# Kernel tuning notes

Hardware: AMD Instinct MI355X
Metric: run time of the kernel (lower is better)

## Reference

```python
import jax, jax.numpy as jnp
import numpy as np

VOCAB = 100000
EMB = 256
HID = 512
H = HID // 2            # per-direction hidden size
T_LEN = 2048
N_TAGS = 7
START, END = 5, 6
NEG = -10000.0


def setup_inputs() -> dict:
    key = jax.random.key(0)
    ks = jax.random.split(key, 16)
    n = lambda k, sh: jax.random.normal(k, sh, dtype=jnp.float32)
    bound = 1.0 / np.sqrt(H)  # torch LSTM/Linear-style init scale
    u = lambda k, sh: jax.random.uniform(k, sh, dtype=jnp.float32, minval=-bound, maxval=bound)
    transitions = n(ks[12], (N_TAGS, N_TAGS))
    transitions = transitions.at[:, START].set(NEG).at[END, :].set(NEG)
    return {
        "words": jax.random.randint(ks[0], (T_LEN,), 0, VOCAB),
        "embed": n(ks[1], (VOCAB + 1, EMB)),
        "W_ih_f": u(ks[2], (4 * H, EMB)),
        "W_hh_f": u(ks[3], (4 * H, H)),
        "b_ih_f": u(ks[4], (4 * H,)),
        "b_hh_f": u(ks[5], (4 * H,)),
        "W_ih_b": u(ks[6], (4 * H, EMB)),
        "W_hh_b": u(ks[7], (4 * H, H)),
        "b_ih_b": u(ks[8], (4 * H,)),
        "b_hh_b": u(ks[9], (4 * H,)),
        "W_out": u(ks[10], (N_TAGS, HID)),
        "b_out": u(ks[11], (N_TAGS,)),
        "transitions": transitions,
        "h0": n(ks[13], (2, H)),
        "c0": n(ks[14], (2, H)),
    }


def _lstm_dir(xs, h0, c0, Wih, Whh, bih, bhh):
    # xs: [T, EMB]; torch gate order i, f, g, o
    def step(carry, x):
        h, c = carry
        g = x @ Wih.T + bih + h @ Whh.T + bhh  # [4H]
        i, f, gg, o = jnp.split(g, 4)
        i, f, o = jax.nn.sigmoid(i), jax.nn.sigmoid(f), jax.nn.sigmoid(o)
        c = f * c + i * jnp.tanh(gg)
        h = o * jnp.tanh(c)
        return (h, c), h
    _, hs = jax.lax.scan(step, (h0, c0), xs)
    return hs  # [T, H]


def _features(words, embed, W_ih_f, W_hh_f, b_ih_f, b_hh_f,
              W_ih_b, W_hh_b, b_ih_b, b_hh_b, W_out, b_out, h0, c0):
    xs = embed[words]                                   # [T, EMB]
    hs_f = _lstm_dir(xs, h0[0], c0[0], W_ih_f, W_hh_f, b_ih_f, b_hh_f)
    hs_b = _lstm_dir(xs[::-1], h0[1], c0[1], W_ih_b, W_hh_b, b_ih_b, b_hh_b)[::-1]
    lstm_out = jnp.concatenate([hs_f, hs_b], axis=1)    # [T, HID]
    return lstm_out @ W_out.T + b_out                   # [T, N_TAGS]


def _viterbi(feats, transitions):
    init = jnp.full((N_TAGS,), NEG, dtype=feats.dtype).at[START].set(0.0)

    def vit_step(fv, feat):
        # torch code: next_tag_var[j] = forward_var + transitions[j]
        M = fv[None, :] + transitions          # [j, i] = fv[i] + T[j, i]
        bp = jnp.argmax(M, axis=1)             # [N_TAGS] best prev tag
        fv_new = jnp.max(M, axis=1) + feat
        return fv_new, bp

    fv, bptrs = jax.lax.scan(vit_step, init, feats)     # bptrs: [T, N_TAGS]
    terminal = fv + transitions[END]
    final_tag = jnp.argmax(terminal)
    path_score = terminal[final_tag]

    def back_step(tag, bp):
        return bp[tag], tag
    _start, path = jax.lax.scan(back_step, final_tag, bptrs, reverse=True)
    return path_score, path  # path: [T] tag ids (B/I/E/S/N = 0..4)


def reference(words, embed, W_ih_f, W_hh_f, b_ih_f, b_hh_f,
              W_ih_b, W_hh_b, b_ih_b, b_hh_b, W_out, b_out,
              transitions, h0, c0):
    feats = _features(words, embed, W_ih_f, W_hh_f, b_ih_f, b_hh_f,
                      W_ih_b, W_hh_b, b_ih_b, b_hh_b, W_out, b_out, h0, c0)
    return _viterbi(feats, transitions)
```

## Files before the change

kernel.cpp:

```cpp
#include <hip/hip_runtime.h>

typedef unsigned int u32;

#define T_LEN 2048
#define NEG (-10000.0f)
#define WSCALE 2032.0f
#define HSCALE 127.0f
#define SCALE_INV (1.0f / (2032.0f * 127.0f))

__device__ __forceinline__ int sdot4(u32 a, u32 b, int c) {
#if __has_builtin(__builtin_amdgcn_sdot4)
  return __builtin_amdgcn_sdot4((int)a, (int)b, c, false);
#else
  int r = c;
  r += (int)(signed char)(a)       * (int)(signed char)(b);
  r += (int)(signed char)(a >> 8)  * (int)(signed char)(b >> 8);
  r += (int)(signed char)(a >> 16) * (int)(signed char)(b >> 16);
  r += (int)(signed char)(a >> 24) * (int)(signed char)(b >> 24);
  return r;
#endif
}

__device__ __forceinline__ u32 rdlane_u32(u32 v, int lane) {
#if __has_builtin(__builtin_amdgcn_readlane)
  return (u32)__builtin_amdgcn_readlane((int)v, lane);
#else
  return (u32)__shfl((int)v, lane);
#endif
}

__device__ __forceinline__ float rdlane_f32(float v, int lane) {
  return __builtin_bit_cast(float, rdlane_u32(__builtin_bit_cast(u32, v), lane));
}

__global__ void pack_whh_i8(const float* __restrict__ Wf,
                            const float* __restrict__ Wb,
                            u32* __restrict__ WP) {
  int idx = blockIdx.x * 256 + threadIdx.x;
  int d   = idx >> 16;
  int rem = idx & 65535;
  int q   = rem >> 12;
  int r   = (rem >> 2) & 1023;
  int j   = rem & 3;
  const float* W = d ? Wb : Wf;
  float4 v = *(const float4*)&W[r * 256 + q * 16 + j * 4];
  int b0 = (int)rintf(fminf(fmaxf(v.x * WSCALE, -127.f), 127.f));
  int b1 = (int)rintf(fminf(fmaxf(v.y * WSCALE, -127.f), 127.f));
  int b2 = (int)rintf(fminf(fmaxf(v.z * WSCALE, -127.f), 127.f));
  int b3 = (int)rintf(fminf(fmaxf(v.w * WSCALE, -127.f), 127.f));
  WP[((d * 16 + q) * 1024 + r) * 4 + j] =
      (u32)(b0 & 255) | ((u32)(b1 & 255) << 8) |
      ((u32)(b2 & 255) << 16) | ((u32)(b3 & 255) << 24);
}

__global__ void gather_kernel(const int* __restrict__ words,
                              const float* __restrict__ embed,
                              float* __restrict__ xs) {
  int t = blockIdx.x;
  int k = threadIdx.x;
  xs[t * 256 + k] = embed[(size_t)words[t] * 256 + k];
}

__global__ __launch_bounds__(256) void gemm_xw(
    const float* __restrict__ xs,
    const float* __restrict__ Wf, const float* __restrict__ Wb,
    const float* __restrict__ bihf, const float* __restrict__ bhhf,
    const float* __restrict__ bihb, const float* __restrict__ bhhb,
    float* __restrict__ XW) {
  __shared__ float lx[32 * 256];
  __shared__ float lw[32 * 132];
  const int tid = threadIdx.x;
  const int t0 = blockIdx.x * 32;
  const int g0 = blockIdx.y * 128;
  const int d  = blockIdx.z;
  const float* W = d ? Wb : Wf;

  #pragma unroll 4
  for (int r = 0; r < 32; ++r) lx[r * 256 + tid] = xs[(t0 + r) * 256 + tid];

  const int tg = tid & 31, tt = tid >> 5;
  float acc[4][4] = {};

  for (int kc = 0; kc < 8; ++kc) {
    __syncthreads();
    #pragma unroll
    for (int r2 = 0; r2 < 16; ++r2) {
      int gg = r2 * 8 + (tid >> 5);
      int k  = tid & 31;
      lw[k * 132 + gg] = W[(g0 + gg) * 256 + kc * 32 + k];
    }
    __syncthreads();
    #pragma unroll
    for (int k = 0; k < 32; ++k) {
      float4 wv = *(const float4*)&lw[k * 132 + tg * 4];
      #pragma unroll
      for (int a = 0; a < 4; ++a) {
        float xa = lx[(tt * 4 + a) * 256 + kc * 32 + k];
        acc[a][0] = fmaf(xa, wv.x, acc[a][0]);
        acc[a][1] = fmaf(xa, wv.y, acc[a][1]);
        acc[a][2] = fmaf(xa, wv.z, acc[a][2]);
        acc[a][3] = fmaf(xa, wv.w, acc[a][3]);
      }
    }
  }
  const float* bih = d ? bihb : bihf;
  const float* bhh = d ? bhhb : bhhf;
  int gcol = g0 + tg * 4;
  float4 bb;
  bb.x = bih[gcol + 0] + bhh[gcol + 0];
  bb.y = bih[gcol + 1] + bhh[gcol + 1];
  bb.z = bih[gcol + 2] + bhh[gcol + 2];
  bb.w = bih[gcol + 3] + bhh[gcol + 3];
  #pragma unroll
  for (int a = 0; a < 4; ++a) {
    float4 o;
    o.x = acc[a][0] + bb.x;
    o.y = acc[a][1] + bb.y;
    o.z = acc[a][2] + bb.z;
    o.w = acc[a][3] + bb.w;
    *(float4*)&XW[((size_t)d * T_LEN + t0 + tt * 4 + a) * 1024 + gcol] = o;
  }
}

__global__ void __launch_bounds__(512)
__attribute__((amdgpu_waves_per_eu(2, 2)))
lstm_seq(
    const float* __restrict__ XW, float* __restrict__ HS,
    const u32* __restrict__ wpack,
    const float* __restrict__ h0, const float* __restrict__ c0) {
  __shared__ u32   H8[64];
  __shared__ float GT[1024];
  const int tid = threadIdx.x;
  const int d = blockIdx.x;
  const int lane = tid & 63;

  uint4 w0[16], w1[16];
  const uint4* wr = (const uint4*)wpack;
  #pragma unroll
  for (int q = 0; q < 16; ++q) {
    w0[q] = wr[(d * 16 + q) * 1024 + tid];
    w1[q] = wr[(d * 16 + q) * 1024 + tid + 512];
  }

  float c = 0.0f, h = 0.0f;
  if (tid < 256) {
    c = c0[d * 256 + tid];
    h = h0[d * 256 + tid];
    int hi = (int)rintf(fminf(fmaxf(h, -1.0f), 1.0f) * HSCALE);
    int h1v = __shfl_down(hi, 1);
    int h2v = __shfl_down(hi, 2);
    int h3v = __shfl_down(hi, 3);
    if (!(tid & 3))
      H8[tid >> 2] = (u32)(hi & 255) | ((u32)(h1v & 255) << 8) |
                     ((u32)(h2v & 255) << 16) | ((u32)(h3v & 255) << 24);
  }
  __syncthreads();
  u32 hA = H8[lane];

  const int delta = d ? -1024 : 1024;
  const float* xwp = XW + ((size_t)d * T_LEN + (d ? (T_LEN - 1) : 0)) * 1024 + tid;
  float xw0c = xwp[0], xw1c = xwp[512];

  for (int s = 0; s < T_LEN; ++s) {
    float xw0n = 0.0f, xw1n = 0.0f;
    if (s < T_LEN - 1) { xwp += delta; xw0n = xwp[0]; xw1n = xwp[512]; }

    int a0 = 0, b0 = 0;
    int a1 = 0, b1 = 0;
    #pragma unroll
    for (int q = 0; q < 16; ++q) {
      u32 s0 = rdlane_u32(hA, 4 * q + 0);
      u32 s1 = rdlane_u32(hA, 4 * q + 1);
      u32 s2 = rdlane_u32(hA, 4 * q + 2);
      u32 s3 = rdlane_u32(hA, 4 * q + 3);
      a0 = sdot4(w0[q].x, s0, a0);
      a1 = sdot4(w1[q].x, s0, a1);
      b0 = sdot4(w0[q].y, s1, b0);
      b1 = sdot4(w1[q].y, s1, b1);
      a0 = sdot4(w0[q].z, s2, a0);
      a1 = sdot4(w1[q].z, s2, a1);
      b0 = sdot4(w0[q].w, s3, b0);
      b1 = sdot4(w1[q].w, s3, b1);
    }
    GT[tid]       = fmaf((float)(a0 + b0), SCALE_INV, xw0c);
    GT[tid + 512] = fmaf((float)(a1 + b1), SCALE_INV, xw1c);
    __syncthreads();

    const int t = d ? (T_LEN - 1 - s) : s;
    if (tid < 256) {
      float gi = GT[tid];
      float gf = GT[256 + tid];
      float gc = GT[512 + tid];
      float go = GT[768 + tid];
      gi = 1.0f / (1.0f + __expf(-gi));
      gf = 1.0f / (1.0f + __expf(-gf));
      go = 1.0f / (1.0f + __expf(-go));
      gc = 1.0f - 2.0f / (__expf(2.0f * gc) + 1.0f);
      c = gf * c + gi * gc;
      float th = 1.0f - 2.0f / (__expf(2.0f * c) + 1.0f);
      h = go * th;
      HS[((size_t)d * T_LEN + t) * 256 + tid] = h;
      int hi = (int)rintf(h * HSCALE);
      int h1v = __shfl_down(hi, 1);
      int h2v = __shfl_down(hi, 2);
      int h3v = __shfl_down(hi, 3);
      if (!(tid & 3))
        H8[tid >> 2] = (u32)(hi & 255) | ((u32)(h1v & 255) << 8) |
                       ((u32)(h2v & 255) << 16) | ((u32)(h3v & 255) << 24);
    }
    __syncthreads();
    hA = H8[lane];
    xw0c = xw0n;
    xw1c = xw1n;
  }
}

__global__ void feats_kernel(const float* __restrict__ hs,
                             const float* __restrict__ wout,
                             const float* __restrict__ bout,
                             float* __restrict__ feats) {
  __shared__ float lf[16 * 257];
  __shared__ float lb[16 * 257];
  const int tid = threadIdx.x;
  const int t0 = blockIdx.x * 16;
  for (int i = tid; i < 16 * 256; i += 128) {
    int r = i >> 8, k = i & 255;
    lf[r * 257 + k] = hs[(size_t)(t0 + r) * 256 + k];
    lb[r * 257 + k] = hs[(size_t)T_LEN * 256 + (size_t)(t0 + r) * 256 + k];
  }
  __syncthreads();
  const int tl = tid >> 3, n = tid & 7;
  if (n < 7) {
    float acc = bout[n];
    #pragma unroll 8
    for (int k = 0; k < 256; ++k) acc = fmaf(lf[tl * 257 + k], wout[n * 512 + k], acc);
    #pragma unroll 8
    for (int k = 0; k < 256; ++k) acc = fmaf(lb[tl * 257 + k], wout[n * 512 + 256 + k], acc);
    feats[(t0 + tl) * 7 + n] = acc;
  }
}

__global__ __launch_bounds__(256) void viterbi_kernel(
    const float* __restrict__ feats,
    const float* __restrict__ trans,
    float* __restrict__ out) {
  extern __shared__ char vsm[];
  float*         fe = (float*)vsm;
  unsigned char* bp = (unsigned char*)(vsm + 57344);
  unsigned char* G  = (unsigned char*)(vsm + 73728);
  unsigned char* bt = (unsigned char*)(vsm + 73984);
  const int tid = threadIdx.x;

  for (int i = tid; i < T_LEN * 7; i += 256) fe[i] = feats[i];
  __syncthreads();

  if (tid < 64) {
    const int j  = tid;
    const int jc = (j < 7) ? j : 0;
    float Trow[7];
    #pragma unroll
    for (int i = 0; i < 7; ++i) Trow[i] = trans[jc * 7 + i];
    float fv = (j == 5) ? 0.0f : NEG;
    for (int t = 0; t < T_LEN; ++t) {
      float f0 = rdlane_f32(fv, 0), f1 = rdlane_f32(fv, 1), f2 = rdlane_f32(fv, 2),
            f3 = rdlane_f32(fv, 3), f4 = rdlane_f32(fv, 4), f5 = rdlane_f32(fv, 5),
            f6 = rdlane_f32(fv, 6);
      float v0 = f0 + Trow[0], v1 = f1 + Trow[1], v2 = f2 + Trow[2],
            v3 = f3 + Trow[3], v4 = f4 + Trow[4], v5 = f5 + Trow[5],
            v6 = f6 + Trow[6];
      bool c01 = v0 >= v1;  float m01 = c01 ? v0 : v1;  int i01 = c01 ? 0 : 1;
      bool c23 = v2 >= v3;  float m23 = c23 ? v2 : v3;  int i23 = c23 ? 2 : 3;
      bool c45 = v4 >= v5;  float m45 = c45 ? v4 : v5;  int i45 = c45 ? 4 : 5;
      bool cA  = m01 >= m23; float mA = cA ? m01 : m23; int iA = cA ? i01 : i23;
      bool cB  = m45 >= v6;  float mB = cB ? m45 : v6;  int iB = cB ? i45 : 6;
      bool cF  = mA >= mB;   float best = cF ? mA : mB; int bi = cF ? iA : iB;
      if (j < 7) bp[t * 8 + j] = (unsigned char)bi;
      fv = best + fe[t * 7 + jc];
    }
    float term = fv + trans[42 + jc];
    float best = rdlane_f32(term, 0); int btag = 0;
    #pragma unroll
    for (int i = 1; i < 7; ++i) {
      float ti = rdlane_f32(term, i);
      if (ti > best) { best = ti; btag = i; }
    }
    if (j == 0) {
      out[0] = best;
      bt[31] = (unsigned char)btag;
    }
  }
  __syncthreads();

  {
    const int s = tid >> 3, j = tid & 7;
    if (s < 32 && j < 7) {
      int g = j;
      for (int t = s * 64 + 63; t >= s * 64; --t) g = bp[t * 8 + g];
      G[s * 8 + j] = (unsigned char)g;
    }
  }
  __syncthreads();

  if (tid == 0) {
    int x = bt[31];
    for (int s = 31; s >= 1; --s) { x = G[s * 8 + x]; bt[s - 1] = (unsigned char)x; }
  }
  __syncthreads();

  if (tid < 32) {
    const int s = tid;
    int tag = bt[s];
    for (int t = s * 64 + 63; t >= s * 64; --t) {
      out[1 + t] = (float)tag;
      tag = bp[t * 8 + tag];
    }
  }
}

extern "C" void kernel_launch(void* const* d_in, const int* in_sizes, int n_in,
                              void* d_out, int out_size, void* d_ws, size_t ws_size,
                              hipStream_t stream) {
  const int*   words = (const int*)d_in[0];
  const float* embed = (const float*)d_in[1];
  const float* Wih_f = (const float*)d_in[2];
  const float* Whh_f = (const float*)d_in[3];
  const float* bih_f = (const float*)d_in[4];
  const float* bhh_f = (const float*)d_in[5];
  const float* Wih_b = (const float*)d_in[6];
  const float* Whh_b = (const float*)d_in[7];
  const float* bih_b = (const float*)d_in[8];
  const float* bhh_b = (const float*)d_in[9];
  const float* Wout  = (const float*)d_in[10];
  const float* bout  = (const float*)d_in[11];
  const float* trans = (const float*)d_in[12];
  const float* h0    = (const float*)d_in[13];
  const float* c0    = (const float*)d_in[14];

  float* ws = (float*)d_ws;
  float* XW = ws;
  float* HS = ws + 4194304;
  float* XS = ws + 5242880;
  float* FE = ws + 5767168;
  u32*   WP = (u32*)(ws + 5781504);

  pack_whh_i8<<<512, 256, 0, stream>>>(Whh_f, Whh_b, WP);
  gather_kernel<<<T_LEN, 256, 0, stream>>>(words, embed, XS);
  dim3 ggrid(T_LEN / 32, 1024 / 128, 2);
  gemm_xw<<<ggrid, 256, 0, stream>>>(XS, Wih_f, Wih_b, bih_f, bhh_f, bih_b, bhh_b, XW);
  lstm_seq<<<2, 512, 0, stream>>>(XW, HS, WP, h0, c0);
  feats_kernel<<<128, 128, 0, stream>>>(HS, Wout, bout, FE);
  viterbi_kernel<<<1, 256, 74048, stream>>>(FE, trans, (float*)d_out);
}
```

Before: 2.615 ms.

## Use byte LDS stores for h, inline-asm dot4 with SGPR operand, lighter barriers

Replaces the three shuffle-down ops and packing with direct per-thread byte stores into the shared int8 h buffer. The dot products become inline v_dot4_i32_i8 with the broadcast h word as a scalar operand, and readlanes are software-pipelined one group ahead. __syncthreads is replaced by an explicit lgkmcnt wait plus s_barrier so the barrier does not also wait on outstanding global (vmcnt) loads and stores. Together these shorten the serial per-timestep critical path of the recurrent loop, at the risk of the asm constraints limiting compiler scheduling.

```diff
diff --git a/kernel.cpp b/kernel.cpp
--- a/kernel.cpp
+++ b/kernel.cpp
@@ -8,18 +8,8 @@
 #define HSCALE 127.0f
 #define SCALE_INV (1.0f / (2032.0f * 127.0f))
 
-__device__ __forceinline__ int sdot4(u32 a, u32 b, int c) {
-#if __has_builtin(__builtin_amdgcn_sdot4)
-  return __builtin_amdgcn_sdot4((int)a, (int)b, c, false);
-#else
-  int r = c;
-  r += (int)(signed char)(a)       * (int)(signed char)(b);
-  r += (int)(signed char)(a >> 8)  * (int)(signed char)(b >> 8);
-  r += (int)(signed char)(a >> 16) * (int)(signed char)(b >> 16);
-  r += (int)(signed char)(a >> 24) * (int)(signed char)(b >> 24);
-  return r;
-#endif
-}
+#define DOT(acc, w, hs) \
+  asm("v_dot4_i32_i8 %0, %2, %1, %0" : "+v"(acc) : "v"(w), "s"(hs))
 
 __device__ __forceinline__ u32 rdlane_u32(u32 v, int lane) {
 #if __has_builtin(__builtin_amdgcn_readlane)
@@ -31,6 +21,11 @@
 
 __device__ __forceinline__ float rdlane_f32(float v, int lane) {
   return __builtin_bit_cast(float, rdlane_u32(__builtin_bit_cast(u32, v), lane));
+}
+
+__device__ __forceinline__ void block_sync_lds() {
+  asm volatile("s_waitcnt lgkmcnt(0)" ::: "memory");
+  __builtin_amdgcn_s_barrier();
 }
 
 __global__ void pack_whh_i8(const float* __restrict__ Wf,
@@ -147,14 +142,9 @@
     c = c0[d * 256 + tid];
     h = h0[d * 256 + tid];
     int hi = (int)rintf(fminf(fmaxf(h, -1.0f), 1.0f) * HSCALE);
-    int h1v = __shfl_down(hi, 1);
-    int h2v = __shfl_down(hi, 2);
-    int h3v = __shfl_down(hi, 3);
-    if (!(tid & 3))
-      H8[tid >> 2] = (u32)(hi & 255) | ((u32)(h1v & 255) << 8) |
-                     ((u32)(h2v & 255) << 16) | ((u32)(h3v & 255) << 24);
-  }
-  __syncthreads();
+    ((unsigned char*)H8)[tid] = (unsigned char)(hi & 255);
+  }
+  block_sync_lds();
   u32 hA = H8[lane];
 
   const int delta = d ? -1024 : 1024;
@@ -167,24 +157,34 @@
 
     int a0 = 0, b0 = 0;
     int a1 = 0, b1 = 0;
-    #pragma unroll
-    for (int q = 0; q < 16; ++q) {
-      u32 s0 = rdlane_u32(hA, 4 * q + 0);
-      u32 s1 = rdlane_u32(hA, 4 * q + 1);
-      u32 s2 = rdlane_u32(hA, 4 * q + 2);
-      u32 s3 = rdlane_u32(hA, 4 * q + 3);
-      a0 = sdot4(w0[q].x, s0, a0);
-      a1 = sdot4(w1[q].x, s0, a1);
-      b0 = sdot4(w0[q].y, s1, b0);
-      b1 = sdot4(w1[q].y, s1, b1);
-      a0 = sdot4(w0[q].z, s2, a0);
-      a1 = sdot4(w1[q].z, s2, a1);
-      b0 = sdot4(w0[q].w, s3, b0);
-      b1 = sdot4(w1[q].w, s3, b1);
+    {
+      u32 s0 = rdlane_u32(hA, 0);
+      u32 s1 = rdlane_u32(hA, 1);
+      u32 s2 = rdlane_u32(hA, 2);
+      u32 s3 = rdlane_u32(hA, 3);
+      #pragma unroll
+      for (int q = 0; q < 16; ++q) {
+        u32 n0 = 0, n1 = 0, n2 = 0, n3 = 0;
+        if (q < 15) {
+          n0 = rdlane_u32(hA, 4 * q + 4);
+          n1 = rdlane_u32(hA, 4 * q + 5);
+          n2 = rdlane_u32(hA, 4 * q + 6);
+          n3 = rdlane_u32(hA, 4 * q + 7);
+        }
+        DOT(a0, w0[q].x, s0);
+        DOT(a1, w1[q].x, s0);
+        DOT(b0, w0[q].y, s1);
+        DOT(b1, w1[q].y, s1);
+        DOT(a0, w0[q].z, s2);
+        DOT(a1, w1[q].z, s2);
+        DOT(b0, w0[q].w, s3);
+        DOT(b1, w1[q].w, s3);
+        s0 = n0; s1 = n1; s2 = n2; s3 = n3;
+      }
     }
     GT[tid]       = fmaf((float)(a0 + b0), SCALE_INV, xw0c);
     GT[tid + 512] = fmaf((float)(a1 + b1), SCALE_INV, xw1c);
-    __syncthreads();
+    block_sync_lds();
 
     const int t = d ? (T_LEN - 1 - s) : s;
     if (tid < 256) {
@@ -201,14 +201,9 @@
       h = go * th;
       HS[((size_t)d * T_LEN + t) * 256 + tid] = h;
       int hi = (int)rintf(h * HSCALE);
-      int h1v = __shfl_down(hi, 1);
-      int h2v = __shfl_down(hi, 2);
-      int h3v = __shfl_down(hi, 3);
-      if (!(tid & 3))
-        H8[tid >> 2] = (u32)(hi & 255) | ((u32)(h1v & 255) << 8) |
-                       ((u32)(h2v & 255) << 16) | ((u32)(h3v & 255) << 24);
-    }
-    __syncthreads();
+      ((unsigned char*)H8)[tid] = (unsigned char)(hi & 255);
+    }
+    block_sync_lds();
     hA = H8[lane];
     xw0c = xw0n;
     xw1c = xw1n;
```

Result: no change. 2.569 ms (-1.8%).
